# Performance work log

Hardware: AMD Instinct MI355X
Metric: run time of the kernel (lower is better)

Reference implementation:

```python
import jax, jax.numpy as jnp
import numpy as np

N_HEAD, D_MODEL, D_HEAD = 16, 1024, 64
SEQ, BSZ = 2048, 4
LN_EPS = 1e-5
SCALE = 1.0 / D_HEAD ** 0.5


def layer_norm(x, gamma, beta):
    m = jnp.mean(x, axis=-1, keepdims=True)
    v = jnp.mean(jnp.square(x - m), axis=-1, keepdims=True)
    return (x - m) * jax.lax.rsqrt(v + LN_EPS) * gamma + beta


def setup_inputs() -> dict:
    key = jax.random.key(0)
    k1, k2, k3, k4, k5, k6 = jax.random.split(key, 6)
    h = jax.random.normal(k1, (SEQ, BSZ, D_MODEL), dtype=jnp.float32)
    attn_mask = jax.random.bernoulli(k2, 0.1, (SEQ, BSZ))
    s = 1.0 / np.sqrt(D_MODEL)
    Wq = jax.random.normal(k3, (D_MODEL, N_HEAD * D_HEAD), dtype=jnp.float32) * s
    Wkv = jax.random.normal(k4, (D_MODEL, 2 * N_HEAD * D_HEAD), dtype=jnp.float32) * s
    Wo = jax.random.normal(k5, (N_HEAD * D_HEAD, D_MODEL), dtype=jnp.float32) * s
    gamma = jnp.ones((D_MODEL,), dtype=jnp.float32)
    beta = jnp.zeros((D_MODEL,), dtype=jnp.float32)
    return {"h": h, "attn_mask": attn_mask, "Wq": Wq, "Wkv": Wkv,
            "Wo": Wo, "gamma": gamma, "beta": beta}


def reference(h, attn_mask, Wq, Wkv, Wo, gamma, beta):
    # h: [S, B, D]; post-LN variant (pre_lnorm=False), mems=None so c == h
    S, B, _ = h.shape
    head_q = (h @ Wq).reshape(S, B, N_HEAD, D_HEAD)
    kv = h @ Wkv
    head_k, head_v = jnp.split(kv, 2, axis=-1)
    head_k = head_k.reshape(S, B, N_HEAD, D_HEAD)
    head_v = head_v.reshape(S, B, N_HEAD, D_HEAD)
    # scores [qlen, klen, B, n]
    attn_score = jnp.einsum('ibnd,jbnd->ijbn', head_q, head_k) * SCALE
    # 2D mask [klen, B] broadcast as [1, klen, B, 1]
    attn_score = jnp.where(attn_mask[None, :, :, None], -jnp.inf, attn_score)
    attn_prob = jax.nn.softmax(attn_score, axis=1)
    attn_vec = jnp.einsum('ijbn,jbnd->ibnd', attn_prob, head_v)
    attn_vec = attn_vec.reshape(S, B, N_HEAD * D_HEAD)
    attn_out = attn_vec @ Wo
    return layer_norm(h + attn_out, gamma, beta)
```

## Files before the change

### kernel.cpp

```cpp
#include <hip/hip_runtime.h>
#include <stdint.h>

#define SEQ 2048
#define BSZ 4
#define NHEAD 16
#define DHEAD 64
#define DMODEL 1024
#define NHD (NHEAD * DHEAD)
#define KVSTR (2 * NHD)

typedef unsigned short u16;
typedef unsigned char u8;
typedef unsigned int u32;
typedef float v4f __attribute__((ext_vector_type(4)));
typedef short v8s __attribute__((ext_vector_type(8)));
typedef u32 v4u __attribute__((ext_vector_type(4)));
typedef u32 v2u __attribute__((ext_vector_type(2)));

#define MASK_NEG 30000.0f
#define BF16_ONES_PAIR 0x3F803F80u

__device__ __forceinline__ float bf2f(u16 h) { return __uint_as_float(((u32)h) << 16); }
__device__ __forceinline__ u16 f2bf(float f) {
  u32 u = __float_as_uint(f);
  return (u16)((u + 0x7fffu + ((u >> 16) & 1u)) >> 16);
}
__device__ __forceinline__ v4f v4f_zero() {
  v4f z; z[0] = 0.f; z[1] = 0.f; z[2] = 0.f; z[3] = 0.f; return z;
}
__device__ __forceinline__ bool is_bf16_mode(const u32* gprobe) {
  return *gprobe == BF16_ONES_PAIR;
}
__device__ __forceinline__ u32 pack_bf16_trunc(float a, float b) {
  return __builtin_amdgcn_perm(__float_as_uint(b), __float_as_uint(a), 0x07060302u);
}

typedef __attribute__((address_space(3))) u32 lds_u32_t;
typedef const __attribute__((address_space(1))) u32 g_u32_t;
__device__ __forceinline__ void async_cp16(const u16* gp, u16* lp) {
  __builtin_amdgcn_global_load_lds((g_u32_t*)gp, (lds_u32_t*)lp, 16, 0, 0);
}

__global__ __launch_bounds__(256) void cast_h(
    const void* __restrict__ src, const u32* __restrict__ gprobe,
    u16* __restrict__ dst) {
  bool bf = is_bf16_mode(gprobe);
  int i4 = blockIdx.x * 256 + threadIdx.x;
  if (bf) {
    ((v2u*)dst)[i4] = ((const v2u*)src)[i4];
  } else {
    v4f v = ((const v4f*)src)[i4];
    v2u o;
    o[0] = (u32)f2bf(v[0]) | ((u32)f2bf(v[1]) << 16);
    o[1] = (u32)f2bf(v[2]) | ((u32)f2bf(v[3]) << 16);
    ((v2u*)dst)[i4] = o;
  }
}

__global__ __launch_bounds__(256) void transpose_w3(
    const void* __restrict__ Wq, const void* __restrict__ Wkv,
    const void* __restrict__ Wo, const u32* __restrict__ gprobe,
    u16* __restrict__ WqT, u16* __restrict__ WkvT, u16* __restrict__ WoT) {
  bool bf = is_bf16_mode(gprobe);
  int z = blockIdx.z;
  int C = (z == 1) ? 2048 : 1024;
  if (blockIdx.x * 32 >= (unsigned)C) return;
  const void* src = (z == 0) ? Wq : (z == 1) ? Wkv : Wo;
  u16* outp = (z == 0) ? WqT : (z == 1) ? WkvT : WoT;
  __shared__ u16 tile[32][33];
  int c0 = blockIdx.x * 32, r0 = blockIdx.y * 32;
  int tx = threadIdx.x & 31, ty = threadIdx.x >> 5;
  if (bf) {
    const u16* in = (const u16*)src;
#pragma unroll
    for (int rr = 0; rr < 4; ++rr)
      tile[ty + rr * 8][tx] = in[(r0 + ty + rr * 8) * C + c0 + tx];
  } else {
    const float* in = (const float*)src;
#pragma unroll
    for (int rr = 0; rr < 4; ++rr)
      tile[ty + rr * 8][tx] = f2bf(in[(r0 + ty + rr * 8) * C + c0 + tx]);
  }
  __syncthreads();
#pragma unroll
  for (int rr = 0; rr < 4; ++rr)
    outp[(c0 + ty + rr * 8) * 1024 + r0 + tx] = tile[tx][ty + rr * 8];
}

__global__ __launch_bounds__(256) void build_vt(
    const u16* __restrict__ KV, u16* __restrict__ Vt) {
  __shared__ u16 tile[32][33];
  int bn = blockIdx.z;
  int b = bn >> 4, n = bn & 15;
  int s0 = blockIdx.x * 32, d0 = blockIdx.y * 32;
  int tx = threadIdx.x & 31, ty = threadIdx.x >> 5;
#pragma unroll
  for (int rr = 0; rr < 4; ++rr) {
    int s = s0 + ty + rr * 8;
    tile[ty + rr * 8][tx] = KV[(s * BSZ + b) * KVSTR + NHD + n * DHEAD + d0 + tx];
  }
  __syncthreads();
#pragma unroll
  for (int rr = 0; rr < 4; ++rr) {
    int d = d0 + ty + rr * 8;
    Vt[bn * (DHEAD * SEQ) + d * SEQ + s0 + tx] = tile[tx][ty + rr * 8];
  }
}

__global__ __launch_bounds__(256) void build_maskf(
    const u32* __restrict__ mraw, float* __restrict__ maskf) {
  bool int8mode = false;
  for (int i = 0; i < 64; ++i) {
    u32 v = mraw[i];
    if (v != 0u && v != 1u && v != 0x3F800000u) int8mode = true;
  }
  int idx = blockIdx.x * 256 + threadIdx.x;
  int b = idx >> 11, j = idx & 2047;
  u32 val = int8mode ? (u32)((const u8*)mraw)[j * BSZ + b] : mraw[j * BSZ + b];
  maskf[idx] = val ? -MASK_NEG : 0.0f;
}

__global__ __launch_bounds__(256) void gemm_qkv(
    const u16* __restrict__ A, const u16* __restrict__ Bt,
    u16* __restrict__ Qm, u16* __restrict__ KVm) {
  const int K = 1024;
  __shared__ __align__(16) u16 As[128 * 32];
  __shared__ __align__(16) u16 Bs[128 * 32];
  const int tid = threadIdx.x;
  const int lane = tid & 63, w = tid >> 6;
  const int quad = lane >> 4, l16 = lane & 15;
  const int wm = w >> 1, wn = w & 1;
  const int m0 = blockIdx.y * 128, n0 = blockIdx.x * 128;
  const int qsw = quad ^ ((l16 >> 1) & 3);

  v4f acc[4][4];
#pragma unroll
  for (int i = 0; i < 4; ++i)
#pragma unroll
    for (int j = 0; j < 4; ++j) acc[i][j] = v4f_zero();

  for (int k0 = 0; k0 < K; k0 += 32) {
    __syncthreads();
#pragma unroll
    for (int it = 0; it < 2; ++it) {
      int g = it * 256 + tid;
      int row = g >> 2;
      int c8 = ((g & 3) ^ ((g >> 3) & 3)) * 8;
      async_cp16(A + (size_t)(m0 + row) * K + k0 + c8, As + 8 * g);
      async_cp16(Bt + (size_t)(n0 + row) * K + k0 + c8, Bs + 8 * g);
    }
    __syncthreads();
    v8s a[4], b[4];
#pragma unroll
    for (int i = 0; i < 4; ++i)
      a[i] = *(const v8s*)(As + (wm * 64 + i * 16 + l16) * 32 + qsw * 8);
#pragma unroll
    for (int j = 0; j < 4; ++j)
      b[j] = *(const v8s*)(Bs + (wn * 64 + j * 16 + l16) * 32 + qsw * 8);
#pragma unroll
    for (int i = 0; i < 4; ++i)
#pragma unroll
      for (int j = 0; j < 4; ++j)
        acc[i][j] = __builtin_amdgcn_mfma_f32_16x16x32_bf16(a[i], b[j], acc[i][j], 0, 0, 0);
  }
  u16* dst = (n0 < 1024) ? Qm : KVm;
  int stride = (n0 < 1024) ? 1024 : 2048;
  int coff = (n0 < 1024) ? n0 : n0 - 1024;
#pragma unroll
  for (int i = 0; i < 4; ++i)
#pragma unroll
    for (int j = 0; j < 4; ++j)
#pragma unroll
      for (int r = 0; r < 4; ++r) {
        int row = m0 + wm * 64 + i * 16 + quad * 4 + r;
        int col = coff + wn * 64 + j * 16 + l16;
        dst[(size_t)row * stride + col] = f2bf(acc[i][j][r]);
      }
}

__global__ __launch_bounds__(256) void gemm_bt(
    const u16* __restrict__ A, const u16* __restrict__ Bt,
    u16* __restrict__ Cb, float* __restrict__ Cf, int store_f32,
    int N, int K) {
  __shared__ __align__(16) u16 As[128 * 32];
  __shared__ __align__(16) u16 Bs[128 * 32];
  const int tid = threadIdx.x;
  const int lane = tid & 63, w = tid >> 6;
  const int quad = lane >> 4, l16 = lane & 15;
  const int wm = w >> 1, wn = w & 1;
  const int m0 = blockIdx.y * 128, n0 = blockIdx.x * 128;
  const int qsw = quad ^ ((l16 >> 1) & 3);

  v4f acc[4][4];
#pragma unroll
  for (int i = 0; i < 4; ++i)
#pragma unroll
    for (int j = 0; j < 4; ++j) acc[i][j] = v4f_zero();

  for (int k0 = 0; k0 < K; k0 += 32) {
    __syncthreads();
#pragma unroll
    for (int it = 0; it < 2; ++it) {
      int g = it * 256 + tid;
      int row = g >> 2;
      int c8 = ((g & 3) ^ ((g >> 3) & 3)) * 8;
      async_cp16(A + (size_t)(m0 + row) * K + k0 + c8, As + 8 * g);
      async_cp16(Bt + (size_t)(n0 + row) * K + k0 + c8, Bs + 8 * g);
    }
    __syncthreads();
    v8s a[4], b[4];
#pragma unroll
    for (int i = 0; i < 4; ++i)
      a[i] = *(const v8s*)(As + (wm * 64 + i * 16 + l16) * 32 + qsw * 8);
#pragma unroll
    for (int j = 0; j < 4; ++j)
      b[j] = *(const v8s*)(Bs + (wn * 64 + j * 16 + l16) * 32 + qsw * 8);
#pragma unroll
    for (int i = 0; i < 4; ++i)
#pragma unroll
      for (int j = 0; j < 4; ++j)
        acc[i][j] = __builtin_amdgcn_mfma_f32_16x16x32_bf16(a[i], b[j], acc[i][j], 0, 0, 0);
  }
#pragma unroll
  for (int i = 0; i < 4; ++i)
#pragma unroll
    for (int j = 0; j < 4; ++j)
#pragma unroll
      for (int r = 0; r < 4; ++r) {
        int row = m0 + wm * 64 + i * 16 + quad * 4 + r;
        int col = n0 + wn * 64 + j * 16 + l16;
        if (store_f32) Cf[(size_t)row * N + col] = acc[i][j][r];
        else Cb[(size_t)row * N + col] = f2bf(acc[i][j][r]);
      }
}

__global__ __launch_bounds__(256, 4) void attn(
    const u16* __restrict__ Q, const u16* __restrict__ KV,
    const u16* __restrict__ Vt, const float* __restrict__ maskf,
    u16* __restrict__ AV) {
  __shared__ __align__(16) u16 Ks[2][2 * 64 * 32];
  __shared__ __align__(16) u16 Vs[2][2 * 64 * 32];
  __shared__ u32 Ps32[4][512];

  const int tid = threadIdx.x;
  const int lane = tid & 63, w = tid >> 6;
  const int quad = lane >> 4, l16 = lane & 15;
  const int bn = blockIdx.y;
  const int b = bn >> 4, n = bn & 15;
  const int q0 = blockIdx.x * 128 + w * 16;
  const int swz = l16 >> 1;
  const int qsw = quad ^ ((l16 >> 1) & 3);

  const float SC = 0.125f * 1.44269504088896340736f;

  const int rl = tid >> 2;
  const int cks = (tid & 3) ^ ((tid >> 3) & 3);
  const u16* kb = KV + ((size_t)rl * BSZ + b) * KVSTR + n * DHEAD;
  const u16* vb = Vt + (size_t)bn * (DHEAD * SEQ) + (size_t)rl * SEQ;

#define STAGE_JT(bi, jtn)                                                  \
  do {                                                                     \
    const u16* kp_ = kb + (size_t)(jtn) * (64 * BSZ * KVSTR);              \
    const u16* vp_ = vb + (jtn) * 64;                                      \
    async_cp16(kp_ + cks * 8,      &Ks[bi][8 * tid]);                      \
    async_cp16(kp_ + 32 + cks * 8, &Ks[bi][2048 + 8 * tid]);               \
    async_cp16(vp_ + cks * 8,      &Vs[bi][8 * tid]);                      \
    async_cp16(vp_ + 32 + cks * 8, &Vs[bi][2048 + 8 * tid]);               \
  } while (0)

  v8s qf[2][2];
#pragma unroll
  for (int s = 0; s < 2; ++s)
#pragma unroll
    for (int c = 0; c < 2; ++c)
      qf[s][c] = *(const v8s*)(Q + ((size_t)(q0 + s * 64 + l16) * BSZ + b) * NHD +
                               n * DHEAD + c * 32 + quad * 8);

  float lrow[2] = {0.f, 0.f};
  v4f ot[2][4];
#pragma unroll
  for (int s = 0; s < 2; ++s)
#pragma unroll
    for (int d = 0; d < 4; ++d) ot[s][d] = v4f_zero();

  const float* mrow = maskf + b * SEQ + quad * 4;

  STAGE_JT(0, 0);
  asm volatile("s_waitcnt vmcnt(0)" ::: "memory");
  __syncthreads();

  for (int jt = 0; jt < SEQ / 64; ++jt) {
    const int cur = jt & 1;
    if (jt + 1 < SEQ / 64) STAGE_JT(cur ^ 1, jt + 1);

    v4f mk[4];
#pragma unroll
    for (int t = 0; t < 4; ++t)
      mk[t] = *(const v4f*)(mrow + jt * 64 + t * 16);

    const u16* KsC = Ks[cur];
    const u16* VsC = Vs[cur];

    v4f st[2][4];
#pragma unroll
    for (int t = 0; t < 4; ++t) {
      v8s kf0 = *(const v8s*)(KsC + (t * 16 + l16) * 32 + qsw * 8);
      v8s kf1 = *(const v8s*)(KsC + (2048 + (t * 16 + l16) * 32) + qsw * 8);
#pragma unroll
      for (int s = 0; s < 2; ++s) {
        v4f acc = __builtin_amdgcn_mfma_f32_16x16x32_bf16(kf0, qf[s][0], v4f_zero(), 0, 0, 0);
        st[s][t] = __builtin_amdgcn_mfma_f32_16x16x32_bf16(kf1, qf[s][1], acc, 0, 0, 0);
      }
    }

    union { v4u u; v8s s; } pu[2][2];
#pragma unroll
    for (int s = 0; s < 2; ++s) {
#pragma unroll
      for (int t = 0; t < 4; ++t) {
        v4f msk = mk[t];
        float p0 = exp2f(fmaf(st[s][t][0], SC, msk[0]));
        float p1 = exp2f(fmaf(st[s][t][1], SC, msk[1]));
        float p2 = exp2f(fmaf(st[s][t][2], SC, msk[2]));
        float p3 = exp2f(fmaf(st[s][t][3], SC, msk[3]));
        lrow[s] += (p0 + p1) + (p2 + p3);
        int base = (t >> 1) * 256 + l16 * 16;
        int jd0 = (t & 1) * 8 + quad * 2;
        Ps32[w][base + ((jd0 + 0) ^ swz)] = pack_bf16_trunc(p0, p1);
        Ps32[w][base + ((jd0 + 1) ^ swz)] = pack_bf16_trunc(p2, p3);
      }
      asm volatile("s_waitcnt lgkmcnt(0)" ::: "memory");
#pragma unroll
      for (int c = 0; c < 2; ++c)
#pragma unroll
        for (int m = 0; m < 4; ++m)
          pu[s][c].u[m] = Ps32[w][c * 256 + l16 * 16 + ((quad * 4 + m) ^ swz)];
      asm volatile("s_waitcnt lgkmcnt(0)" ::: "memory");
    }

#pragma unroll
    for (int ds = 0; ds < 4; ++ds)
#pragma unroll
      for (int c = 0; c < 2; ++c) {
        v8s vf = *(const v8s*)(VsC + (c * 64 + ds * 16 + l16) * 32 + qsw * 8);
#pragma unroll
        for (int s = 0; s < 2; ++s)
          ot[s][ds] = __builtin_amdgcn_mfma_f32_16x16x32_bf16(vf, pu[s][c].s, ot[s][ds], 0, 0, 0);
      }

    asm volatile("s_waitcnt vmcnt(0)" ::: "memory");
    __syncthreads();
  }
#undef STAGE_JT

#pragma unroll
  for (int s = 0; s < 2; ++s) {
    float l = lrow[s];
    l += __shfl_xor(l, 16);
    l += __shfl_xor(l, 32);
    float inv = 1.0f / fmaxf(l, 1e-30f);
#pragma unroll
    for (int ds = 0; ds < 4; ++ds)
#pragma unroll
      for (int r = 0; r < 4; ++r) {
        int d = ds * 16 + quad * 4 + r;
        AV[((size_t)(q0 + s * 64 + l16) * BSZ + b) * NHD + n * DHEAD + d] =
            f2bf(ot[s][ds][r] * inv);
      }
  }
}

__global__ __launch_bounds__(256) void add_ln(
    const void* __restrict__ h, const float* __restrict__ AO,
    const void* __restrict__ gamma, const void* __restrict__ beta,
    void* __restrict__ outp) {
  bool bf = is_bf16_mode((const u32*)gamma);
  const int row = blockIdx.x, tid = threadIdx.x;
  const int lane = tid & 63, w = tid >> 6;
  __shared__ float rs1[4], rs2[4];
  const int col = tid * 4;
  v4f av = *(const v4f*)(AO + (size_t)row * DMODEL + col);
  float x[4], g[4], be[4];
  if (bf) {
    v2u hv = ((const v2u*)h)[row * 256 + tid];
    x[0] = bf2f((u16)(hv[0] & 0xffff)) + av[0];
    x[1] = bf2f((u16)(hv[0] >> 16)) + av[1];
    x[2] = bf2f((u16)(hv[1] & 0xffff)) + av[2];
    x[3] = bf2f((u16)(hv[1] >> 16)) + av[3];
    v2u gv = ((const v2u*)gamma)[tid];
    v2u bv = ((const v2u*)beta)[tid];
    g[0] = bf2f((u16)(gv[0] & 0xffff)); g[1] = bf2f((u16)(gv[0] >> 16));
    g[2] = bf2f((u16)(gv[1] & 0xffff)); g[3] = bf2f((u16)(gv[1] >> 16));
    be[0] = bf2f((u16)(bv[0] & 0xffff)); be[1] = bf2f((u16)(bv[0] >> 16));
    be[2] = bf2f((u16)(bv[1] & 0xffff)); be[3] = bf2f((u16)(bv[1] >> 16));
  } else {
    v4f hv = ((const v4f*)h)[row * 256 + tid];
    x[0] = hv[0] + av[0]; x[1] = hv[1] + av[1];
    x[2] = hv[2] + av[2]; x[3] = hv[3] + av[3];
    v4f gv = ((const v4f*)gamma)[tid];
    v4f bv = ((const v4f*)beta)[tid];
    g[0] = gv[0]; g[1] = gv[1]; g[2] = gv[2]; g[3] = gv[3];
    be[0] = bv[0]; be[1] = bv[1]; be[2] = bv[2]; be[3] = bv[3];
  }
  float s1 = x[0] + x[1] + x[2] + x[3];
  float s2 = x[0] * x[0] + x[1] * x[1] + x[2] * x[2] + x[3] * x[3];
#pragma unroll
  for (int off = 1; off < 64; off <<= 1) {
    s1 += __shfl_xor(s1, off);
    s2 += __shfl_xor(s2, off);
  }
  if (lane == 0) { rs1[w] = s1; rs2[w] = s2; }
  __syncthreads();
  s1 = rs1[0] + rs1[1] + rs1[2] + rs1[3];
  s2 = rs2[0] + rs2[1] + rs2[2] + rs2[3];
  float mean = s1 * (1.0f / DMODEL);
  float var = s2 * (1.0f / DMODEL) - mean * mean;
  float rstd = rsqrtf(var + 1e-5f);
  float y0 = (x[0] - mean) * rstd * g[0] + be[0];
  float y1 = (x[1] - mean) * rstd * g[1] + be[1];
  float y2 = (x[2] - mean) * rstd * g[2] + be[2];
  float y3 = (x[3] - mean) * rstd * g[3] + be[3];
  if (bf) {
    v2u ov;
    ov[0] = (u32)f2bf(y0) | ((u32)f2bf(y1) << 16);
    ov[1] = (u32)f2bf(y2) | ((u32)f2bf(y3) << 16);
    ((v2u*)outp)[row * 256 + tid] = ov;
  } else {
    v4f ov; ov[0] = y0; ov[1] = y1; ov[2] = y2; ov[3] = y3;
    ((v4f*)outp)[row * 256 + tid] = ov;
  }
}

extern "C" void kernel_launch(void* const* d_in, const int* in_sizes, int n_in,
                              void* d_out, int out_size, void* d_ws, size_t ws_size,
                              hipStream_t stream) {
  const void* h    = d_in[0];
  const u32* mask  = (const u32*)d_in[1];
  const void* Wq   = d_in[2];
  const void* Wkv  = d_in[3];
  const void* Wo   = d_in[4];
  const void* gamma = d_in[5];
  const void* beta  = d_in[6];
  const u32* gprobe = (const u32*)gamma;

  char* ws = (char*)d_ws;
  const size_t MB = 1 << 20;
  u16* hb      = (u16*)(ws + 0 * MB);
  u16* Vtm     = (u16*)(ws + 0 * MB);
  u16* KVm     = (u16*)(ws + 16 * MB);
  float* AOm   = (float*)(ws + 16 * MB);
  u16* WqT     = (u16*)(ws + 48 * MB);
  u16* WkvT    = (u16*)(ws + 50 * MB);
  u16* WoT     = (u16*)(ws + 54 * MB);
  float* maskf = (float*)(ws + 56 * MB);
  u16* Qm      = (u16*)d_out;

  cast_h<<<dim3(8192), 256, 0, stream>>>(h, gprobe, hb);
  transpose_w3<<<dim3(64, 32, 3), 256, 0, stream>>>(Wq, Wkv, Wo, gprobe, WqT, WkvT, WoT);
  build_maskf<<<dim3((SEQ * BSZ) / 256), 256, 0, stream>>>(mask, maskf);

  gemm_qkv<<<dim3(24, 64), 256, 0, stream>>>(hb, WqT, Qm, KVm);

  build_vt<<<dim3(64, 2, 64), 256, 0, stream>>>(KVm, Vtm);

  attn<<<dim3(16, 64), 256, 0, stream>>>(Qm, KVm, Vtm, maskf, Qm);

  gemm_bt<<<dim3(8, 64), 256, 0, stream>>>(Qm, WoT, nullptr, AOm, 1, 1024, 1024);
  add_ln<<<dim3(8192), 256, 0, stream>>>(h, AOm, gamma, beta, d_out);
}
```

Before: 349.1 us.

## Feed softmax probabilities to PV MFMA directly from registers, skipping LDS

The attention kernel no longer round-trips the bf16 probability tile through a per-wave LDS buffer. The packed P values stay in registers in the layout the score MFMA produced. The V fragment reads are reorganised into two 8-byte LDS loads per MFMA so that the reduction index matches that register layout. This removes LDS stores and loads plus two lgkmcnt waits per key tile, at the cost of more, smaller V LDS reads.

```diff
diff --git a/kernel.cpp b/kernel.cpp
--- a/kernel.cpp
+++ b/kernel.cpp
@@ -14,6 +14,7 @@
 typedef unsigned int u32;
 typedef float v4f __attribute__((ext_vector_type(4)));
 typedef short v8s __attribute__((ext_vector_type(8)));
+typedef short v4s __attribute__((ext_vector_type(4)));
 typedef u32 v4u __attribute__((ext_vector_type(4)));
 typedef u32 v2u __attribute__((ext_vector_type(2)));
 
@@ -240,7 +241,6 @@
     u16* __restrict__ AV) {
   __shared__ __align__(16) u16 Ks[2][2 * 64 * 32];
   __shared__ __align__(16) u16 Vs[2][2 * 64 * 32];
-  __shared__ u32 Ps32[4][512];
 
   const int tid = threadIdx.x;
   const int lane = tid & 63, w = tid >> 6;
@@ -248,7 +248,6 @@
   const int bn = blockIdx.y;
   const int b = bn >> 4, n = bn & 15;
   const int q0 = blockIdx.x * 128 + w * 16;
-  const int swz = l16 >> 1;
   const int qsw = quad ^ ((l16 >> 1) & 3);
 
   const float SC = 0.125f * 1.44269504088896340736f;
@@ -285,6 +284,11 @@
 
   const float* mrow = maskf + b * SEQ + quad * 4;
 
+  const int vsub = (quad & 1) * 4;
+  const int vxor = (l16 >> 1) & 3;
+  const int vc0 = (((quad >> 1) + 0) ^ vxor) * 8 + vsub;
+  const int vc1 = (((quad >> 1) + 2) ^ vxor) * 8 + vsub;
+
   STAGE_JT(0, 0);
   asm volatile("s_waitcnt vmcnt(0)" ::: "memory");
   __syncthreads();
@@ -313,9 +317,10 @@
       }
     }
 
-    union { v4u u; v8s s; } pu[2][2];
-#pragma unroll
-    for (int s = 0; s < 2; ++s) {
+    union PU { v4u u; v8s s; };
+    PU pf[2][2];
+#pragma unroll
+    for (int s = 0; s < 2; ++s)
 #pragma unroll
       for (int t = 0; t < 4; ++t) {
         v4f msk = mk[t];
@@ -324,29 +329,23 @@
         float p2 = exp2f(fmaf(st[s][t][2], SC, msk[2]));
         float p3 = exp2f(fmaf(st[s][t][3], SC, msk[3]));
         lrow[s] += (p0 + p1) + (p2 + p3);
-        int base = (t >> 1) * 256 + l16 * 16;
-        int jd0 = (t & 1) * 8 + quad * 2;
-        Ps32[w][base + ((jd0 + 0) ^ swz)] = pack_bf16_trunc(p0, p1);
-        Ps32[w][base + ((jd0 + 1) ^ swz)] = pack_bf16_trunc(p2, p3);
-      }
-      asm volatile("s_waitcnt lgkmcnt(0)" ::: "memory");
-#pragma unroll
-      for (int c = 0; c < 2; ++c)
-#pragma unroll
-        for (int m = 0; m < 4; ++m)
-          pu[s][c].u[m] = Ps32[w][c * 256 + l16 * 16 + ((quad * 4 + m) ^ swz)];
-      asm volatile("s_waitcnt lgkmcnt(0)" ::: "memory");
+        pf[s][t >> 1].u[(t & 1) * 2 + 0] = pack_bf16_trunc(p0, p1);
+        pf[s][t >> 1].u[(t & 1) * 2 + 1] = pack_bf16_trunc(p2, p3);
+      }
+
+#pragma unroll
+    for (int tp = 0; tp < 2; ++tp) {
+#pragma unroll
+      for (int ds = 0; ds < 4; ++ds) {
+        union VU { v4s h[2]; v8s v; } vf;
+        const int rb = tp * 2048 + (ds * 16 + l16) * 32;
+        vf.h[0] = *(const v4s*)(VsC + rb + vc0);
+        vf.h[1] = *(const v4s*)(VsC + rb + vc1);
+#pragma unroll
+        for (int s = 0; s < 2; ++s)
+          ot[s][ds] = __builtin_amdgcn_mfma_f32_16x16x32_bf16(vf.v, pf[s][tp].s, ot[s][ds], 0, 0, 0);
+      }
     }
-
-#pragma unroll
-    for (int ds = 0; ds < 4; ++ds)
-#pragma unroll
-      for (int c = 0; c < 2; ++c) {
-        v8s vf = *(const v8s*)(VsC + (c * 64 + ds * 16 + l16) * 32 + qsw * 8);
-#pragma unroll
-        for (int s = 0; s < 2; ++s)
-          ot[s][ds] = __builtin_amdgcn_mfma_f32_16x16x32_bf16(vf, pu[s][c].s, ot[s][ds], 0, 0, 0);
-      }
 
     asm volatile("s_waitcnt vmcnt(0)" ::: "memory");
     __syncthreads();
```

Result: faster. 339.5 us (-2.7%).
